# Performance work log

Measured on AMD Instinct MI355X. Metric: run time of the kernel, lower is better.

Reference implementation:

```python
import jax, jax.numpy as jnp
import numpy as np

HIDDEN = 1024
HEADS = 16
HEAD_DIM = HIDDEN // HEADS
LN_EPS = 1e-12


def _layer_norm(x, gamma, beta, eps=LN_EPS):
    mu = jnp.mean(x, axis=-1, keepdims=True)
    var = jnp.var(x, axis=-1, keepdims=True)
    return (x - mu) * jax.lax.rsqrt(var + eps) * gamma + beta


def setup_inputs() -> dict:
    key = jax.random.key(0)
    ks = jax.random.split(key, 8)
    B, S = 4, 2048
    hidden_states = jax.random.normal(ks[0], (B, S, HIDDEN), dtype=jnp.float32)
    attention_mask = jnp.zeros((B, 1, 1, S), dtype=jnp.float32)
    scale = 1.0 / np.sqrt(HIDDEN)
    return {
        "hidden_states": hidden_states,
        "attention_mask": attention_mask,
        "ln_gamma": jnp.ones((HIDDEN,), jnp.float32),
        "ln_beta": jnp.zeros((HIDDEN,), jnp.float32),
        "W_qkv": jax.random.normal(ks[1], (HIDDEN, 3 * HIDDEN), jnp.float32) * scale,
        "b_qkv": jnp.zeros((3 * HIDDEN,), jnp.float32),
        "W_out": jax.random.normal(ks[2], (HIDDEN, HIDDEN), jnp.float32) * scale,
        "b_out": jnp.zeros((HIDDEN,), jnp.float32),
    }


def reference(hidden_states, attention_mask, ln_gamma, ln_beta, W_qkv, b_qkv, W_out, b_out):
    B, S, H = hidden_states.shape
    x = _layer_norm(hidden_states, ln_gamma, ln_beta)
    qkv = x @ W_qkv + b_qkv  # [B, S, 3H]
    q, k, v = jnp.split(qkv, 3, axis=-1)
    q = q.reshape(B, S, HEADS, HEAD_DIM)
    k = k.reshape(B, S, HEADS, HEAD_DIM)
    v = v.reshape(B, S, HEADS, HEAD_DIM)
    # scores: [B, heads, q_len, kv_len]
    scores = jnp.einsum("bqhd,bkhd->bhqk", q, k) * (1.0 / np.sqrt(HEAD_DIM))
    scores = scores + attention_mask
    probs = jax.nn.softmax(scores, axis=-1)
    attn = jnp.einsum("bhqk,bkhd->bqhd", probs, v).reshape(B, S, H)
    out = attn @ W_out + b_out
    out = out + hidden_states  # residual (dropout is identity at p=0)
    return out
```

## Files before the change

kernel.cpp:

```cpp
#include <hip/hip_runtime.h>

#define SEQ 2048
#define HID 1024
#define NHEAD 16
#define HDIM 64
#define NB 4
#define NTOK (NB * SEQ)
#define NQKV (3 * HID)
#define LOG2E 1.44269504088896f
#define QSCALE (0.125f * LOG2E)

typedef __attribute__((ext_vector_type(8))) short bf16x8;
typedef __attribute__((ext_vector_type(4))) float f32x4;


__device__ __forceinline__ void glds16(const void* g, void* l) {
  __builtin_amdgcn_global_load_lds(
      (const __attribute__((address_space(1))) void*)g,
      (__attribute__((address_space(3))) void*)l, 16, 0, 0);
}

__device__ __forceinline__ ushort f2bf(float f) {
  union { float f; unsigned int u; } a; a.f = f;
  unsigned int u = a.u;
  return (ushort)((u + 0x7fffu + ((u >> 16) & 1u)) >> 16);
}

__device__ __forceinline__ unsigned int cvtpk(float a, float b) {
  unsigned int r;
  asm("v_cvt_pk_bf16_f32 %0, %1, %2" : "=v"(r) : "v"(a), "v"(b));
  return r;
}


__global__ __launch_bounds__(256) void ln_tr_fused(const float* __restrict__ x,
                                                   const float* __restrict__ g,
                                                   const float* __restrict__ be,
                                                   ushort* __restrict__ y,
                                                   const float* __restrict__ W0,
                                                   ushort* __restrict__ T0,
                                                   const float* __restrict__ W1,
                                                   ushort* __restrict__ T1,
                                                   const float* __restrict__ mask,
                                                   float* __restrict__ m2) {
  __shared__ float t[32][33];
  const int tid = threadIdx.x;
  if (blockIdx.x < NTOK) {
    const int row = blockIdx.x;
    const float4 v = ((const float4*)(x + (size_t)row * HID))[tid];
    float s  = v.x + v.y + v.z + v.w;
    float sq = v.x * v.x + v.y * v.y + v.z * v.z + v.w * v.w;
    for (int o = 1; o < 64; o <<= 1) { s += __shfl_xor(s, o, 64); sq += __shfl_xor(sq, o, 64); }
    const int wv = tid >> 6;
    if ((tid & 63) == 0) { t[0][wv] = s; t[1][wv] = sq; }
    __syncthreads();
    s  = t[0][0] + t[0][1] + t[0][2] + t[0][3];
    sq = t[1][0] + t[1][1] + t[1][2] + t[1][3];
    const float mu  = s * (1.0f / HID);
    const float var = sq * (1.0f / HID) - mu * mu;
    const float rs  = rsqrtf(var + 1e-12f);
    const float4 gv = ((const float4*)g)[tid];
    const float4 bv = ((const float4*)be)[tid];
    ushort4 o;
    o.x = f2bf((v.x - mu) * rs * gv.x + bv.x);
    o.y = f2bf((v.y - mu) * rs * gv.y + bv.y);
    o.z = f2bf((v.z - mu) * rs * gv.z + bv.z);
    o.w = f2bf((v.w - mu) * rs * gv.w + bv.w);
    ((ushort4*)(y + (size_t)row * HID))[tid] = o;
    return;
  }
  const int bid = blockIdx.x - NTOK;
  if (bid >= 4096) {
    const int i = (bid - 4096) * 1024 + tid * 4;
    float4 v = *(const float4*)(mask + i);
    v.x *= LOG2E; v.y *= LOG2E; v.z *= LOG2E; v.w *= LOG2E;
    *(float4*)(m2 + i) = v;
    return;
  }
  const float* W; ushort* WT; int C, bx, by;
  if (bid < 3072) { W = W0; WT = T0; C = NQKV; bx = bid % 96; by = bid / 96; }
  else { const int b2 = bid - 3072; W = W1; WT = T1; C = HID; bx = b2 & 31; by = b2 >> 5; }
  const int R = HID;
  const int c0 = bx * 32, r0 = by * 32;
  const int tx = tid & 31, ty = tid >> 5;
  for (int j = 0; j < 4; ++j)
    t[ty + j * 8][tx] = W[(size_t)(r0 + ty + j * 8) * C + c0 + tx];
  __syncthreads();
  for (int j = 0; j < 4; ++j)
    WT[(size_t)(c0 + ty + j * 8) * R + r0 + tx] = f2bf(t[tx][ty + j * 8]);
}


__global__ __launch_bounds__(256) void v_transpose(const ushort* __restrict__ qkv,
                                                   ushort* __restrict__ vt) {
  __shared__ ushort t[64][66];
  const int s0 = blockIdx.x * 64, h = blockIdx.y, b = blockIdx.z;
  const size_t tokbase = (size_t)b * SEQ;
  for (int e = 0; e < 2; ++e) {
    const int c = e * 256 + threadIdx.x;
    const int sr = c >> 3, dc = c & 7;
    *(uint4*)&t[sr][dc * 8] =
        *(const uint4*)(qkv + (tokbase + s0 + sr) * NQKV + 2 * HID + h * HDIM + dc * 8);
  }
  __syncthreads();
  for (int e = 0; e < 2; ++e) {
    const int c = e * 256 + threadIdx.x;
    const int dr = c >> 3, sc = c & 7;
    ushort tmp[8];
    for (int j = 0; j < 8; ++j) tmp[j] = t[sc * 8 + j][dr];
    *(uint4*)(vt + ((size_t)(b * NHEAD + h) * HDIM + dr) * SEQ + s0 + sc * 8) = *(uint4*)tmp;
  }
}


template <int MODE>
__global__ __launch_bounds__(256) void gemm_bt(const ushort* __restrict__ A,
                                               const ushort* __restrict__ Bt,
                                               const float* __restrict__ bias,
                                               const float* __restrict__ resid,
                                               ushort* __restrict__ obf,
                                               float* __restrict__ of32,
                                               ushort* __restrict__ vtob,
                                               int M, int N, int K) {
  __shared__ ushort As[128 * 64];
  __shared__ ushort Bs[128 * 64];
  const int tid = threadIdx.x;
  const int lane = tid & 63, wv = tid >> 6;
  const int q = lane >> 4, li = lane & 15;
  const int nwgx = gridDim.x;
  const int hw = blockIdx.x + nwgx * blockIdx.y;
  const int cpx = (nwgx * gridDim.y) >> 3;
  const int logical = (hw & 7) * cpx + (hw >> 3);
  const int bx = logical % nwgx, by = logical / nwgx;
  const int m0 = by * 128, n0 = bx * 128;
  const int wm = (wv >> 1) * 64, wn = (wv & 1) * 64;
  f32x4 acc[4][4] = {};

  for (int kb = 0; kb < K; kb += 64) {
    for (int e = 0; e < 4; ++e) {
      const int chunk = (wv * 4 + e) * 64 + lane;
      const int row = chunk >> 3, slot = chunk & 7;
      const int kc = slot ^ (row & 7);
      glds16(A  + (size_t)(m0 + row) * K + kb + kc * 8, As + (wv * 4 + e) * 512);
      glds16(Bt + (size_t)(n0 + row) * K + kb + kc * 8, Bs + (wv * 4 + e) * 512);
    }
    __syncthreads();
    for (int ks = 0; ks < 2; ++ks) {
      const int kc = ks * 4 + q;
      bf16x8 af[4], bfr[4];
      for (int mi = 0; mi < 4; ++mi) {
        const int row = wm + mi * 16 + li;
        af[mi] = *(const bf16x8*)(As + (row * 8 + (kc ^ (row & 7))) * 8);
      }
      for (int ni = 0; ni < 4; ++ni) {
        const int row = wn + ni * 16 + li;
        bfr[ni] = *(const bf16x8*)(Bs + (row * 8 + (kc ^ (row & 7))) * 8);
      }
      for (int mi = 0; mi < 4; ++mi)
        for (int ni = 0; ni < 4; ++ni)
          acc[mi][ni] = __builtin_amdgcn_mfma_f32_16x16x32_bf16(af[mi], bfr[ni], acc[mi][ni], 0, 0, 0);
    }
    __syncthreads();
  }

  if (MODE == 0 && vtob != nullptr && n0 >= 2 * HID) {
    const int b = (m0 + wm) >> 11;
    const int sbase = (m0 + wm) & (SEQ - 1);
    for (int ni = 0; ni < 4; ++ni) {
      const int colv = n0 - 2 * HID + wn + ni * 16 + li;
      const int h = colv >> 6, d = colv & 63;
      const float bvs = bias[n0 + wn + ni * 16 + li];
      ushort* vbase = vtob + ((size_t)(b * NHEAD + h) * HDIM + d) * SEQ;
      for (int mi = 0; mi < 4; ++mi) {
        const int s = sbase + mi * 16 + q * 4;
        ushort4 o;
        o.x = f2bf(acc[mi][ni][0] + bvs);
        o.y = f2bf(acc[mi][ni][1] + bvs);
        o.z = f2bf(acc[mi][ni][2] + bvs);
        o.w = f2bf(acc[mi][ni][3] + bvs);
        *(ushort4*)(vbase + s) = o;
      }
    }
    return;
  }

  const float qs = (MODE == 0 && n0 < HID) ? QSCALE : 1.0f;
  for (int ni = 0; ni < 4; ++ni) {
    const int col = n0 + wn + ni * 16 + li;
    const float bvs = bias[col] * qs;
    for (int mi = 0; mi < 4; ++mi) {
      for (int r = 0; r < 4; ++r) {
        const int row = m0 + wm + mi * 16 + q * 4 + r;
        const float v = fmaf(acc[mi][ni][r], qs, bvs);
        if (MODE == 0) obf[(size_t)row * N + col] = f2bf(v);
        else           of32[(size_t)row * N + col] = v + resid[(size_t)row * N + col];
      }
    }
  }
}


template <int PRE>
__global__ __launch_bounds__(512) void flash_attn(const ushort* __restrict__ qkv,
                                                  const ushort* __restrict__ vt,
                                                  const float* __restrict__ mask,
                                                  ushort* __restrict__ outa) {
  __shared__ ushort KV[2][8192];
  const int tid = threadIdx.x, lane = tid & 63, wv = tid >> 6;
  const int quad = lane >> 4, li = lane & 15;
  const int wq = wv * 32;
  constexpr int NT = SEQ / 64;

  const int L = blockIdx.x + 8 * blockIdx.y + 128 * blockIdx.z;
  const int xcd = L & 7, rrem = L >> 3;
  const int p = (rrem >> 3) * 8 + xcd;
  const int qt0 = rrem & 7, h = p & 15, b = p >> 4;

  const size_t tokbase = (size_t)b * SEQ;
  const size_t vtbase = (size_t)(b * NHEAD + h) * HDIM * SEQ;
  const float* mrow = mask + (size_t)b * SEQ;

  for (int e = 0; e < 4; ++e) {
    const int c = (wv * 4 + e) * 64 + lane;
    const int row = c >> 3, slot = c & 7;
    const int kc = slot ^ (row & 7);
    const int gtok = qt0 * 128 + (row & 127) + (row >> 7) * 1024;
    glds16(qkv + (tokbase + gtok) * NQKV + h * HDIM + kc * 8,
           &KV[0][0] + (wv * 4 + e) * 512);
  }
  __syncthreads();

  bf16x8 qf[2][2];
  for (int ks = 0; ks < 2; ++ks) {
    const int kc = ks * 4 + quad;
    for (int nq = 0; nq < 2; ++nq) {
      const int row = wq + nq * 16 + li;
      qf[ks][nq] = *(const bf16x8*)(&KV[0][0] + (row * 8 + (kc ^ (row & 7))) * 8);
    }
  }
  __syncthreads();

  int koff[2][4], voff[2][4];
  for (int ks = 0; ks < 2; ++ks) {
    const int kc = ks * 4 + quad;
    for (int i = 0; i < 4; ++i) {
      const int row = i * 16 + li;
      koff[ks][i] = (row * 8 + (kc ^ (row & 7))) * 8;
      voff[ks][i] = koff[ks][i] + 4096;
    }
  }
  unsigned ksoff, vsoff;
  {
    const int c = wv * 64 + lane;
    const int row = c >> 3, slot = c & 7;
    const int kc = slot ^ (row & 7);
    const int gkv = (row & 0x23) | ((row & 0x0c) << 1) | ((row & 0x10) >> 2);
    ksoff = (unsigned)((tokbase + gkv) * NQKV + HID + h * HDIM + kc * 8);
    vsoff = (unsigned)(vtbase + (size_t)row * SEQ + kc * 8);
  }

  const unsigned int one2 = 0x3F803F80u;
  bf16x8 ones;
  for (int j = 0; j < 4; ++j) ((unsigned int*)&ones)[j] = one2;

  f32x4 accO[2][4] = {};
  f32x4 accL[2] = {};

  auto stage_kv = [&](int t, int buf) {
    const unsigned ka = (unsigned)(t * (64 * NQKV));
    const unsigned va = (unsigned)(t * 64);
    glds16(qkv + ksoff + ka, &KV[buf][0] + wv * 512);
    glds16(vt + vsoff + va,  &KV[buf][4096] + wv * 512);
  };

  auto mask_fetch = [&](int t, f32x4 (&mk)[4]) {
    const int kv0 = (t & (NT - 1)) * 64;
    for (int m = 0; m < 4; ++m) {
      if (PRE) {
        mk[m] = *(const f32x4*)(mrow + kv0 + (m >> 1) * 32 + quad * 8 + (m & 1) * 4);
      } else {
        const float4 v = *(const float4*)(mrow + kv0 + (m >> 1) * 32 + quad * 8 + (m & 1) * 4);
        mk[m][0] = v.x * LOG2E; mk[m][1] = v.y * LOG2E;
        mk[m][2] = v.z * LOG2E; mk[m][3] = v.w * LOG2E;
      }
    }
  };

  auto compute = [&](int t, int buf, f32x4 (&mkc)[4], f32x4 (&mkn)[4]) {
    mask_fetch(t + 1, mkn);

    const ushort* Kb = &KV[buf][0];

    f32x4 sc[2][4];
    __builtin_amdgcn_s_setprio(1);
    for (int ks = 0; ks < 2; ++ks) {
      bf16x8 kf[4];
      for (int m = 0; m < 4; ++m)
        kf[m] = *(const bf16x8*)(Kb + koff[ks][m]);
      for (int nq = 0; nq < 2; ++nq)
        for (int m = 0; m < 4; ++m)
          sc[nq][m] = __builtin_amdgcn_mfma_f32_16x16x32_bf16(
              kf[m], qf[ks][nq], ks == 0 ? mkc[m] : sc[nq][m], 0, 0, 0);
    }
    __builtin_amdgcn_s_setprio(0);

    for (int ks = 0; ks < 2; ++ks) {
      bf16x8 vf[4];
      for (int nd = 0; nd < 4; ++nd)
        vf[nd] = *(const bf16x8*)(Kb + voff[ks][nd]);
      unsigned int pk[2][2][2];
      for (int nq = 0; nq < 2; ++nq)
        for (int mm = 0; mm < 2; ++mm) {
          const int m = 2 * ks + mm;
          const float p0 = __builtin_amdgcn_exp2f(sc[nq][m][0]);
          const float p1 = __builtin_amdgcn_exp2f(sc[nq][m][1]);
          const float p2 = __builtin_amdgcn_exp2f(sc[nq][m][2]);
          const float p3 = __builtin_amdgcn_exp2f(sc[nq][m][3]);
          pk[nq][mm][0] = cvtpk(p0, p1);
          pk[nq][mm][1] = cvtpk(p2, p3);
        }
      __builtin_amdgcn_s_setprio(1);
      for (int mq = 0; mq < 2; ++mq) {
        bf16x8 pf;
        ((unsigned int*)&pf)[0] = pk[mq][0][0];
        ((unsigned int*)&pf)[1] = pk[mq][0][1];
        ((unsigned int*)&pf)[2] = pk[mq][1][0];
        ((unsigned int*)&pf)[3] = pk[mq][1][1];
        for (int nd = 0; nd < 4; ++nd)
          accO[mq][nd] = __builtin_amdgcn_mfma_f32_16x16x32_bf16(pf, vf[nd], accO[mq][nd], 0, 0, 0);
        accL[mq] = __builtin_amdgcn_mfma_f32_16x16x32_bf16(pf, ones, accL[mq], 0, 0, 0);
      }
      __builtin_amdgcn_s_setprio(0);
    }
  };

  f32x4 mkA[4], mkB[4];
  mask_fetch(0, mkA);
  stage_kv(0, 0);
  for (int t = 0; t < NT; t += 2) {
    __syncthreads();
    stage_kv(t + 1, 1);
    compute(t, 0, mkA, mkB);
    __syncthreads();
    if (t + 2 < SEQ / 64) stage_kv(t + 2, 0);
    compute(t + 1, 1, mkB, mkA);
  }

  for (int mq = 0; mq < 2; ++mq)
    for (int r = 0; r < 4; ++r) {
      const float inv = 1.0f / accL[mq][r];
      const size_t tok = tokbase + qt0 * 128 + ((size_t)(wv >> 2) << 10) +
                         (wv & 3) * 32 + mq * 16 + quad * 4 + r;
      for (int nd = 0; nd < 4; ++nd)
        outa[tok * HID + h * HDIM + nd * 16 + li] = f2bf(accO[mq][nd][r] * inv);
    }
}


extern "C" void kernel_launch(void* const* d_in, const int* in_sizes, int n_in,
                              void* d_out, int out_size, void* d_ws, size_t ws_size,
                              hipStream_t stream) {
  const float* hidden = (const float*)d_in[0];
  const float* mask   = (const float*)d_in[1];
  const float* gamma  = (const float*)d_in[2];
  const float* beta   = (const float*)d_in[3];
  const float* Wqkv   = (const float*)d_in[4];
  const float* bqkv   = (const float*)d_in[5];
  const float* Wout   = (const float*)d_in[6];
  const float* bout   = (const float*)d_in[7];
  float* out = (float*)d_out;

  char* ws = (char*)d_ws;
  const bool fuse_vt = ws_size >= ((size_t)104 << 20);
  const bool pre_msk = ws_size >= (((size_t)104 << 20) + (NB * SEQ * 4 + 65536));
  ushort* x_bf  = (ushort*)(ws);
  ushort* wqkvT = (ushort*)(ws + ((size_t)16 << 20));
  ushort* woutT = (ushort*)(ws + ((size_t)22 << 20));
  ushort* qkvb  = (ushort*)(ws + ((size_t)24 << 20));
  ushort* attnb = (ushort*)(ws + ((size_t)72 << 20));
  ushort* vtb   = fuse_vt ? (ushort*)(ws + ((size_t)88 << 20))
                          : (ushort*)(ws);
  float* m2     = pre_msk ? (float*)(ws + ((size_t)104 << 20)) : nullptr;

  ln_tr_fused<<<NTOK + 4096 + (m2 ? 8 : 0), 256, 0, stream>>>(
      hidden, gamma, beta, x_bf, Wqkv, wqkvT, Wout, woutT, mask, m2);
  gemm_bt<0><<<dim3(NQKV / 128, NTOK / 128), 256, 0, stream>>>(
      x_bf, wqkvT, bqkv, nullptr, qkvb, nullptr, fuse_vt ? vtb : nullptr, NTOK, NQKV, HID);
  if (!fuse_vt)
    v_transpose<<<dim3(SEQ / 64, NHEAD, NB), 256, 0, stream>>>(qkvb, vtb);
  if (m2)
    flash_attn<1><<<dim3(SEQ / 256, NHEAD, NB), 512, 0, stream>>>(qkvb, vtb, m2, attnb);
  else
    flash_attn<0><<<dim3(SEQ / 256, NHEAD, NB), 512, 0, stream>>>(qkvb, vtb, mask, attnb);
  gemm_bt<1><<<dim3(HID / 128, NTOK / 128), 256, 0, stream>>>(
      attnb, woutT, bout, hidden, nullptr, out, nullptr, NTOK, HID, HID);
}
```

Measured before the change: 280.6 us.

## Halve query rows per attention block to double the grid size

Each flash-attention block now handles 128 query rows (16 per wave) instead of 256 (32 per wave), and the grid doubles to 1024 blocks, with the XCD-aware block remapping adjusted to match. This lowers per-wave register use and gives more blocks to spread across CUs. In exchange, K/V tiles are loaded from global/LDS twice as often per query row and each wave issues fewer MFMAs per K/V fragment load.

```diff
diff --git a/kernel.cpp b/kernel.cpp
--- a/kernel.cpp
+++ b/kernel.cpp
@@ -208,35 +208,31 @@
   __shared__ ushort KV[2][8192];
   const int tid = threadIdx.x, lane = tid & 63, wv = tid >> 6;
   const int quad = lane >> 4, li = lane & 15;
-  const int wq = wv * 32;
   constexpr int NT = SEQ / 64;
 
-  const int L = blockIdx.x + 8 * blockIdx.y + 128 * blockIdx.z;
+  const int L = blockIdx.x + 16 * blockIdx.y + 256 * blockIdx.z;
   const int xcd = L & 7, rrem = L >> 3;
-  const int p = (rrem >> 3) * 8 + xcd;
-  const int qt0 = rrem & 7, h = p & 15, b = p >> 4;
+  const int p = (rrem >> 4) * 8 + xcd;
+  const int qt = rrem & 15, h = p & 15, b = p >> 4;
 
   const size_t tokbase = (size_t)b * SEQ;
   const size_t vtbase = (size_t)(b * NHEAD + h) * HDIM * SEQ;
   const float* mrow = mask + (size_t)b * SEQ;
 
-  for (int e = 0; e < 4; ++e) {
-    const int c = (wv * 4 + e) * 64 + lane;
+  for (int e = 0; e < 2; ++e) {
+    const int c = (wv * 2 + e) * 64 + lane;
     const int row = c >> 3, slot = c & 7;
     const int kc = slot ^ (row & 7);
-    const int gtok = qt0 * 128 + (row & 127) + (row >> 7) * 1024;
-    glds16(qkv + (tokbase + gtok) * NQKV + h * HDIM + kc * 8,
-           &KV[0][0] + (wv * 4 + e) * 512);
+    glds16(qkv + (tokbase + qt * 128 + row) * NQKV + h * HDIM + kc * 8,
+           &KV[0][0] + (wv * 2 + e) * 512);
   }
   __syncthreads();
 
-  bf16x8 qf[2][2];
+  bf16x8 qf[2];
   for (int ks = 0; ks < 2; ++ks) {
     const int kc = ks * 4 + quad;
-    for (int nq = 0; nq < 2; ++nq) {
-      const int row = wq + nq * 16 + li;
-      qf[ks][nq] = *(const bf16x8*)(&KV[0][0] + (row * 8 + (kc ^ (row & 7))) * 8);
-    }
+    const int row = wv * 16 + li;
+    qf[ks] = *(const bf16x8*)(&KV[0][0] + (row * 8 + (kc ^ (row & 7))) * 8);
   }
   __syncthreads();
 
@@ -263,8 +259,8 @@
   bf16x8 ones;
   for (int j = 0; j < 4; ++j) ((unsigned int*)&ones)[j] = one2;
 
-  f32x4 accO[2][4] = {};
-  f32x4 accL[2] = {};
+  f32x4 accO[4] = {};
+  f32x4 accL = {};
 
   auto stage_kv = [&](int t, int buf) {
     const unsigned ka = (unsigned)(t * (64 * NQKV));
@@ -291,16 +287,15 @@
 
     const ushort* Kb = &KV[buf][0];
 
-    f32x4 sc[2][4];
+    f32x4 sc[4];
     __builtin_amdgcn_s_setprio(1);
     for (int ks = 0; ks < 2; ++ks) {
       bf16x8 kf[4];
       for (int m = 0; m < 4; ++m)
         kf[m] = *(const bf16x8*)(Kb + koff[ks][m]);
-      for (int nq = 0; nq < 2; ++nq)
-        for (int m = 0; m < 4; ++m)
-          sc[nq][m] = __builtin_amdgcn_mfma_f32_16x16x32_bf16(
-              kf[m], qf[ks][nq], ks == 0 ? mkc[m] : sc[nq][m], 0, 0, 0);
+      for (int m = 0; m < 4; ++m)
+        sc[m] = __builtin_amdgcn_mfma_f32_16x16x32_bf16(
+            kf[m], qf[ks], ks == 0 ? mkc[m] : sc[m], 0, 0, 0);
     }
     __builtin_amdgcn_s_setprio(0);
 
@@ -308,28 +303,25 @@
       bf16x8 vf[4];
       for (int nd = 0; nd < 4; ++nd)
         vf[nd] = *(const bf16x8*)(Kb + voff[ks][nd]);
-      unsigned int pk[2][2][2];
-      for (int nq = 0; nq < 2; ++nq)
-        for (int mm = 0; mm < 2; ++mm) {
-          const int m = 2 * ks + mm;
-          const float p0 = __builtin_amdgcn_exp2f(sc[nq][m][0]);
-          const float p1 = __builtin_amdgcn_exp2f(sc[nq][m][1]);
-          const float p2 = __builtin_amdgcn_exp2f(sc[nq][m][2]);
-          const float p3 = __builtin_amdgcn_exp2f(sc[nq][m][3]);
-          pk[nq][mm][0] = cvtpk(p0, p1);
-          pk[nq][mm][1] = cvtpk(p2, p3);
-        }
+      unsigned int pk[2][2];
+      for (int mm = 0; mm < 2; ++mm) {
+        const int m = 2 * ks + mm;
+        const float p0 = __builtin_amdgcn_exp2f(sc[m][0]);
+        const float p1 = __builtin_amdgcn_exp2f(sc[m][1]);
+        const float p2 = __builtin_amdgcn_exp2f(sc[m][2]);
+        const float p3 = __builtin_amdgcn_exp2f(sc[m][3]);
+        pk[mm][0] = cvtpk(p0, p1);
+        pk[mm][1] = cvtpk(p2, p3);
+      }
       __builtin_amdgcn_s_setprio(1);
-      for (int mq = 0; mq < 2; ++mq) {
-        bf16x8 pf;
-        ((unsigned int*)&pf)[0] = pk[mq][0][0];
-        ((unsigned int*)&pf)[1] = pk[mq][0][1];
-        ((unsigned int*)&pf)[2] = pk[mq][1][0];
-        ((unsigned int*)&pf)[3] = pk[mq][1][1];
-        for (int nd = 0; nd < 4; ++nd)
-          accO[mq][nd] = __builtin_amdgcn_mfma_f32_16x16x32_bf16(pf, vf[nd], accO[mq][nd], 0, 0, 0);
-        accL[mq] = __builtin_amdgcn_mfma_f32_16x16x32_bf16(pf, ones, accL[mq], 0, 0, 0);
-      }
+      bf16x8 pf;
+      ((unsigned int*)&pf)[0] = pk[0][0];
+      ((unsigned int*)&pf)[1] = pk[0][1];
+      ((unsigned int*)&pf)[2] = pk[1][0];
+      ((unsigned int*)&pf)[3] = pk[1][1];
+      for (int nd = 0; nd < 4; ++nd)
+        accO[nd] = __builtin_amdgcn_mfma_f32_16x16x32_bf16(pf, vf[nd], accO[nd], 0, 0, 0);
+      accL = __builtin_amdgcn_mfma_f32_16x16x32_bf16(pf, ones, accL, 0, 0, 0);
       __builtin_amdgcn_s_setprio(0);
     }
   };
@@ -346,14 +338,12 @@
     compute(t + 1, 1, mkB, mkA);
   }
 
-  for (int mq = 0; mq < 2; ++mq)
-    for (int r = 0; r < 4; ++r) {
-      const float inv = 1.0f / accL[mq][r];
-      const size_t tok = tokbase + qt0 * 128 + ((size_t)(wv >> 2) << 10) +
-                         (wv & 3) * 32 + mq * 16 + quad * 4 + r;
-      for (int nd = 0; nd < 4; ++nd)
-        outa[tok * HID + h * HDIM + nd * 16 + li] = f2bf(accO[mq][nd][r] * inv);
-    }
+  for (int r = 0; r < 4; ++r) {
+    const float inv = 1.0f / accL[r];
+    const size_t tok = tokbase + qt * 128 + wv * 16 + quad * 4 + r;
+    for (int nd = 0; nd < 4; ++nd)
+      outa[tok * HID + h * HDIM + nd * 16 + li] = f2bf(accO[nd][r] * inv);
+  }
 }
 
 
@@ -389,9 +379,9 @@
   if (!fuse_vt)
     v_transpose<<<dim3(SEQ / 64, NHEAD, NB), 256, 0, stream>>>(qkvb, vtb);
   if (m2)
-    flash_attn<1><<<dim3(SEQ / 256, NHEAD, NB), 512, 0, stream>>>(qkvb, vtb, m2, attnb);
+    flash_attn<1><<<dim3(SEQ / 128, NHEAD, NB), 512, 0, stream>>>(qkvb, vtb, m2, attnb);
   else
-    flash_attn<0><<<dim3(SEQ / 256, NHEAD, NB), 512, 0, stream>>>(qkvb, vtb, mask, attnb);
+    flash_attn<0><<<dim3(SEQ / 128, NHEAD, NB), 512, 0, stream>>>(qkvb, vtb, mask, attnb);
   gemm_bt<1><<<dim3(HID / 128, NTOK / 128), 256, 0, stream>>>(
       attnb, woutT, bout, hidden, nullptr, out, nullptr, NTOK, HID, HID);
 }
```

Result: no change. 284.9 us (+1.5%).
